# Performance work log

Hardware: AMD Instinct MI355X
Metric: run time of the kernel (lower is better)

## Reference

```python
import jax, jax.numpy as jnp
import numpy as np

D = 32   # input_dim == all hidden dims
L = 4    # number of GeneralizedRelationalConv layers
R = 36   # num_relation (incl. inverse relations)


def _bellmanford(edge_index, edge_type, h_index, r_index, num_nodes,
                 query_emb, rel_W, rel_b, conv_W, conv_b):
    """NBFNet Bellman-Ford pass: relation-conditioned conv with PNA aggregation."""
    B = r_index.shape[0]
    N = num_nodes
    E = edge_type.shape[0]
    d = query_emb.shape[1]

    query = query_emb[r_index]                                   # [B, d]
    # boundary condition: indicator embedding at the head node
    boundary = jnp.zeros((B, N, d), jnp.float32).at[jnp.arange(B), h_index].add(query)

    src, dst = edge_index[0], edge_index[1]
    # augment every node with a self-loop carrying the boundary message
    idx_aug = jnp.concatenate([dst, jnp.arange(N)])              # [E + N]
    deg = jax.ops.segment_sum(jnp.ones(E + N, jnp.float32), idx_aug, num_segments=N)  # >= 1
    dlog = jnp.log(deg)
    scale = dlog / jnp.mean(dlog)
    # PNA degree scalers: identity / amplification / attenuation
    scales = jnp.stack([jnp.ones_like(scale), scale, 1.0 / jnp.clip(scale, 1e-2)], axis=-1)  # [N, 3]

    x = boundary
    for l in range(L):
        # dependent relation embeddings: linear projection of the query
        rel = (query @ rel_W[l].T + rel_b[l]).reshape(B, R, d)   # [B, R, d]
        # distmult message: gather source state, modulate by edge relation
        msg = x[:, src, :] * rel[:, edge_type, :]                # [B, E, d]
        msg = jnp.concatenate([msg, boundary], axis=1)           # [B, E+N, d] incl. self-loops

        def agg(m):  # segment stats over destination nodes
            s = jax.ops.segment_sum(m, idx_aug, num_segments=N)
            sq = jax.ops.segment_sum(m * m, idx_aug, num_segments=N)
            mx = jax.ops.segment_max(m, idx_aug, num_segments=N)
            mn = jax.ops.segment_min(m, idx_aug, num_segments=N)
            return s, sq, mx, mn

        s, sq, mx, mn = jax.vmap(agg)(msg)                       # each [B, N, d]
        mean = s / deg[:, None]
        sq_mean = sq / deg[:, None]
        std = jnp.sqrt(jnp.clip(sq_mean - mean * mean, 1e-6))
        feats = jnp.stack([mean, mx, mn, std], axis=-1).reshape(B, N, 4 * d)
        update = (feats[..., None] * scales[None, :, None, :]).reshape(B, N, 12 * d)
        # combine: linear over cat(input, pna_update) then ReLU
        x = jax.nn.relu(jnp.concatenate([x, update], axis=-1) @ conv_W[l].T + conv_b[l])

    node_query = jnp.broadcast_to(query[:, None, :], (B, N, d))
    return jnp.concatenate([x, node_query], axis=-1)             # [B, N, 2d]


def setup_inputs() -> dict:
    key = jax.random.key(0)
    ks = jax.random.split(key, 10)
    N, E, B, K = 20000, 200000, 4, 32
    return {
        "edge_index": jax.random.randint(ks[0], (2, E), 0, N),
        "edge_type": jax.random.randint(ks[1], (E,), 0, R),
        "h_index": jax.random.randint(ks[2], (B,), 0, N),
        "t_index": jax.random.randint(ks[3], (B, K), 0, N),
        "r_index": jax.random.randint(ks[4], (B,), 0, R),
        "num_nodes": N,
        "query_emb": jax.random.normal(ks[5], (R, D), jnp.float32) * 0.1,
        "rel_W": jax.random.normal(ks[6], (L, R * D, D), jnp.float32) * 0.1,
        "rel_b": jnp.zeros((L, R * D), jnp.float32),
        "conv_W": jax.random.normal(ks[7], (L, D, 13 * D), jnp.float32) * 0.05,
        "conv_b": jnp.zeros((L, D), jnp.float32),
        "mlp_W1": jax.random.normal(ks[8], (2 * D, 2 * D), jnp.float32) * 0.1,
        "mlp_b1": jnp.zeros((2 * D,), jnp.float32),
        "mlp_W2": jax.random.normal(ks[9], (1, 2 * D), jnp.float32) * 0.1,
        "mlp_b2": jnp.zeros((1,), jnp.float32),
    }


def reference(edge_index, edge_type, h_index, t_index, r_index, num_nodes,
              query_emb, rel_W, rel_b, conv_W, conv_b,
              mlp_W1, mlp_b1, mlp_W2, mlp_b2):
    feature = _bellmanford(edge_index, edge_type, h_index, r_index, num_nodes,
                           query_emb, rel_W, rel_b, conv_W, conv_b)
    B = h_index.shape[0]
    f_t = feature[jnp.arange(B)[:, None], t_index]               # [B, K, 2d]
    h = jax.nn.relu(f_t @ mlp_W1.T + mlp_b1)
    score = (h @ mlp_W2.T + mlp_b2)[..., 0]                      # [B, K]
    return score
```

## Files before the change

kernel.cpp:

```cpp
#include <hip/hip_runtime.h>
#include <hip/hip_bf16.h>

#define N_NODES 20000
#define N_EDGES 200000
#define BB 4
#define KK 32
#define DD 32
#define RR 36
#define LL 4
#define NCHUNKS (N_NODES / 16)
#define NBLK 79

constexpr size_t OFF_X0   = 0;
constexpr size_t OFF_X1   = OFF_X0 + (size_t)BB * N_NODES * DD;
constexpr size_t OFF_RP   = OFF_X1 + (size_t)BB * N_NODES * DD;
constexpr size_t OFF_CUR  = OFF_RP + 20032;
constexpr size_t OFF_ES   = OFF_CUR + N_NODES;
constexpr size_t OFF_DEG  = OFF_ES + N_EDGES;
constexpr size_t OFF_SC   = OFF_DEG + N_NODES;
constexpr size_t OFF_INV  = OFF_SC + N_NODES;
constexpr size_t OFF_BS   = OFF_INV + N_NODES;
constexpr size_t OFF_BL   = OFF_BS + 128;
constexpr size_t OFF_BO   = OFF_BL + 128;
constexpr size_t OFF_MEAN = OFF_BO + 128;
constexpr size_t OFF_REL  = OFF_MEAN + 16;
constexpr size_t OFF_PW   = OFF_REL + (size_t)LL * RR * BB * DD;
constexpr size_t OFF_F    = OFF_PW + (size_t)LL * 16 * 832;


__global__ void k_init(const int* __restrict__ h_index, const int* __restrict__ r_index,
                       const float* __restrict__ query_emb, float* __restrict__ x0,
                       int* __restrict__ cursor) {
    int i = blockIdx.x * blockDim.x + threadIdx.x;
    int stride = gridDim.x * blockDim.x;
    for (int t = i; t < N_NODES; t += stride) cursor[t] = 0;
    for (int t = i; t < BB * N_NODES * DD; t += stride) {
        int b = t & 3; int d = (t >> 2) & 31; int n = t >> 7;
        float v = 0.f;
        if (n == h_index[b]) v = query_emb[r_index[b] * DD + d];
        x0[t] = v;
    }
}

__global__ void k_hist(const int* __restrict__ ei, int* __restrict__ cursor) {
    int e = blockIdx.x * blockDim.x + threadIdx.x;
    if (e < N_EDGES) atomicAdd(&cursor[ei[N_EDGES + e]], 1);
}

__global__ void k_part(const int* __restrict__ cursor, int* __restrict__ bsum,
                       float* __restrict__ blog) {
    __shared__ int si[256];
    __shared__ float sf2[256];
    int tid = threadIdx.x;
    int i = blockIdx.x * 256 + tid;
    int v = (i < N_NODES) ? cursor[i] : 0;
    float lg = (i < N_NODES) ? logf((float)(v + 1)) : 0.f;
    si[tid] = v; sf2[tid] = lg;
    __syncthreads();
    for (int off = 128; off > 0; off >>= 1) {
        if (tid < off) { si[tid] += si[tid + off]; sf2[tid] += sf2[tid + off]; }
        __syncthreads();
    }
    if (tid == 0) { bsum[blockIdx.x] = si[0]; blog[blockIdx.x] = sf2[0]; }
}

__global__ void k_scan2(const int* __restrict__ bsum, const float* __restrict__ blog,
                        int* __restrict__ boff, float* __restrict__ meanw) {
    __shared__ int si[128];
    __shared__ float sf2[128];
    int t = threadIdx.x;
    int v = (t < NBLK) ? bsum[t] : 0;
    float lg = (t < NBLK) ? blog[t] : 0.f;
    si[t] = v; sf2[t] = lg;
    __syncthreads();
    for (int off = 1; off < 128; off <<= 1) {
        int tv = (t >= off) ? si[t - off] : 0;
        float tf = (t >= off) ? sf2[t - off] : 0.f;
        __syncthreads();
        si[t] += tv; sf2[t] += tf;
        __syncthreads();
    }
    if (t < NBLK) boff[t] = si[t] - v;
    if (t == 127) meanw[0] = sf2[127] / (float)N_NODES;
}

__global__ void k_final(int* __restrict__ cursor, int* __restrict__ row_ptr,
                        const int* __restrict__ boff, const float* __restrict__ meanw,
                        float* __restrict__ rdeg, float* __restrict__ scale,
                        float* __restrict__ invs) {
    __shared__ int si[256];
    int tid = threadIdx.x;
    int i = blockIdx.x * 256 + tid;
    int v = (i < N_NODES) ? cursor[i] : 0;
    si[tid] = v;
    __syncthreads();
    for (int off = 1; off < 256; off <<= 1) {
        int tv = (tid >= off) ? si[tid - off] : 0;
        __syncthreads();
        si[tid] += tv;
        __syncthreads();
    }
    int rp = boff[blockIdx.x] + si[tid] - v;
    if (i < N_NODES) {
        row_ptr[i] = rp;
        cursor[i] = rp;
        float dg = (float)(v + 1);
        float sc = logf(dg) / meanw[0];
        rdeg[i] = 1.f / dg;
        scale[i] = sc;
        invs[i] = 1.f / fmaxf(sc, 0.01f);
    }
    if (i == 0) row_ptr[N_NODES] = N_EDGES;
}

__global__ void k_scatter(const int* __restrict__ ei, const int* __restrict__ et,
                          int* __restrict__ cursor, int* __restrict__ es) {
    int e = blockIdx.x * blockDim.x + threadIdx.x;
    if (e < N_EDGES) {
        int dnode = ei[N_EDGES + e];
        int p = atomicAdd(&cursor[dnode], 1);
        es[p] = ei[e] | (et[e] << 16);
    }
}

__global__ void k_prep_w(const float* __restrict__ query_emb, const int* __restrict__ r_index,
                         const float* __restrict__ rel_W, const float* __restrict__ rel_b,
                         const float* __restrict__ conv_W,
                         float* __restrict__ rel_all, float* __restrict__ pw) {
    int i = blockIdx.x * blockDim.x + threadIdx.x;
    const int NREL = LL * BB * RR * DD;
    if (i < NREL) {
        int d = i & 31;
        int ty = (i >> 5) % RR;
        int b = (i / (32 * RR)) & 3;
        int l = i / (32 * RR * BB);
        const float* q = query_emb + r_index[b] * DD;
        const float* w = rel_W + ((size_t)l * RR * DD + ty * DD + d) * DD;
        float acc = rel_b[l * RR * DD + ty * DD + d];
        #pragma unroll
        for (int k2 = 0; k2 < DD; ++k2) acc = fmaf(q[k2], w[k2], acc);
        rel_all[(((size_t)l * RR + ty) * DD + d) * BB + b] = acc;
    } else {
        int i2 = i - NREL;
        if (i2 >= LL * 16 * 832) return;
        int r = i2 % 832; int lw = i2 / 832;
        int w = lw & 15, l = lw >> 4;
        int o, col;
        if (r < 64) { col = r >> 1; o = w * 2 + (r & 1); }
        else {
            int r2 = r - 64;
            int jj = r2 / 24, rem = r2 % 24;
            int p = rem >> 1;
            o = w * 2 + (rem & 1);
            col = DD + (jj * 4 + p / 3) * 3 + (p % 3);
        }
        pw[i2] = conv_W[(size_t)(l * DD + o) * (13 * DD) + col];
    }
}

__launch_bounds__(256, 6)
__global__ void k_gather(const float* __restrict__ xin, float4* __restrict__ Fq,
                         const int* __restrict__ row_ptr, const int* __restrict__ es,
                         const float* __restrict__ rel_l, const float* __restrict__ rdeg,
                         const int* __restrict__ h_index, const int* __restrict__ r_index,
                         const float* __restrict__ query_emb) {
    __shared__ __align__(16) float s_rel[RR * BB * DD];
    const int tid = threadIdx.x;
    {
        const float4* p4 = (const float4*)rel_l;
        float4* s4 = (float4*)s_rel;
        for (int i = tid; i < RR * BB * DD / 4; i += 256) s4[i] = p4[i];
    }
    const int lane = tid & 63;
    const int d = lane & 31;
    const int par = lane >> 5;
    int hb[4]; float qv[4];
    #pragma unroll
    for (int b = 0; b < 4; ++b) {
        hb[b] = h_index[b];
        qv[b] = query_emb[r_index[b] * DD + d];
    }
    __syncthreads();

    const int nwaves = gridDim.x * 4;
    for (int n = blockIdx.x * 4 + (tid >> 6); n < N_NODES; n += nwaves) {
        float sa[4], sq[4], mx[4], mn[4];
        #pragma unroll
        for (int b = 0; b < 4; ++b) {
            float bv = (n == hb[b]) ? qv[b] : 0.f;
            float bs = par ? 0.f : bv;
            sa[b] = bs; sq[b] = bs * bv; mx[b] = bv; mn[b] = bv;
        }
        auto proc = [&](int ee) {
            int pk = es[ee];
            float4 xv = *(const float4*)(xin + ((size_t)(pk & 0xFFFF) * DD + d) * 4);
            float4 rv = *(const float4*)(s_rel + (((pk >> 16) * DD) + d) * 4);
            #pragma unroll
            for (int b = 0; b < 4; ++b) {
                float m = (&xv.x)[b] * (&rv.x)[b];
                sa[b] += m; sq[b] = fmaf(m, m, sq[b]);
                mx[b] = fmaxf(mx[b], m); mn[b] = fminf(mn[b], m);
            }
        };
        int e0 = row_ptr[n], e1 = row_ptr[n + 1];
        int e = e0 + par;
        for (; e + 6 < e1; e += 8) { proc(e); proc(e + 2); proc(e + 4); proc(e + 6); }
        for (; e < e1; e += 2) proc(e);
        #pragma unroll
        for (int b = 0; b < 4; ++b) {
            sa[b] += __shfl_xor(sa[b], 32);
            sq[b] += __shfl_xor(sq[b], 32);
            mx[b] = fmaxf(mx[b], __shfl_xor(mx[b], 32));
            mn[b] = fminf(mn[b], __shfl_xor(mn[b], 32));
        }
        float rd_ = rdeg[n];
        float mean[4], sd[4];
        #pragma unroll
        for (int b = 0; b < 4; ++b) {
            mean[b] = sa[b] * rd_;
            float sm = sq[b] * rd_;
            sd[b] = sqrtf(fmaxf(sm - mean[b] * mean[b], 1e-6f));
        }
        const int chunk = n >> 4, nl = n & 15;
        int tA = nl * 4 + par * 2;
        float4 fA, fB;
        fA.x = par ? mean[2] : mean[0]; fA.y = par ? mx[2] : mx[0];
        fA.z = par ? mn[2] : mn[0];     fA.w = par ? sd[2] : sd[0];
        fB.x = par ? mean[3] : mean[1]; fB.y = par ? mx[3] : mx[1];
        fB.z = par ? mn[3] : mn[1];     fB.w = par ? sd[3] : sd[1];
        Fq[(size_t)(chunk * 32 + d) * 64 + tA] = fA;
        Fq[(size_t)(chunk * 32 + d) * 64 + tA + 1] = fB;
    }
}

#define FMAB(CF, JJ) do {                                                      \
    _Pragma("unroll")                                                          \
    for (int p_ = 0; p_ < 12; ++p_) {                                          \
        const int f_ = p_ / 3, k_ = p_ % 3;                                    \
        float wlo_ = wfp[(JJ) * 24 + p_ * 2];                                  \
        float whi_ = wfp[(JJ) * 24 + p_ * 2 + 1];                              \
        _Pragma("unroll")                                                      \
        for (int cc_ = 0; cc_ < 5; ++cc_) {                                    \
            float cv_ = (&CF[cc_].x)[f_];                                      \
            y[cc_][k_][0] = fmaf(cv_, wlo_, y[cc_][k_][0]);                    \
            y[cc_][k_][1] = fmaf(cv_, whi_, y[cc_][k_][1]);                    \
        }                                                                      \
    }                                                                          \
} while (0)

#define LOADCF(CF, ROW) do {                                                   \
    _Pragma("unroll")                                                          \
    for (int cc_ = 0; cc_ < 5; ++cc_)                                          \
        CF[cc_] = Fq[(size_t)((set * 5 + cc_) * 32 + (ROW)) * 64 + lane];      \
} while (0)

__launch_bounds__(1024, 4)
__global__ void k_conv(const float* __restrict__ xin, float* __restrict__ xout,
                       const float4* __restrict__ Fq, const float* __restrict__ pw_l,
                       const float* __restrict__ scale, const float* __restrict__ invs,
                       const float* __restrict__ conv_b_l) {
    const int tid = threadIdx.x;
    const int wq = __builtin_amdgcn_readfirstlane(tid >> 6);
    const int lane = tid & 63;
    const float* wxp = pw_l + wq * 832;
    const float* wfp = wxp + 64;
    float bx = conv_b_l[wq * 2], by = conv_b_l[wq * 2 + 1];

    const int set = blockIdx.x;
    const int nl2 = lane >> 2, b2 = lane & 3;

    float y[5][3][2];
    #pragma unroll
    for (int cc = 0; cc < 5; ++cc) {
        y[cc][0][0] = bx; y[cc][0][1] = by;
        y[cc][1][0] = 0.f; y[cc][1][1] = 0.f;
        y[cc][2][0] = 0.f; y[cc][2][1] = 0.f;
    }

    #pragma unroll 2
    for (int jg = 0; jg < 8; ++jg) {
        float cxv[5][4];
        #pragma unroll
        for (int cc = 0; cc < 5; ++cc) {
            int n = (set * 5 + cc) * 16 + nl2;
            const float* xb = xin + (size_t)n * 128 + b2;
            #pragma unroll
            for (int dj = 0; dj < 4; ++dj)
                cxv[cc][dj] = xb[(jg * 4 + dj) * 4];
        }
        #pragma unroll
        for (int dj = 0; dj < 4; ++dj) {
            int j = jg * 4 + dj;
            float wlo = wxp[2 * j];
            float whi = wxp[2 * j + 1];
            #pragma unroll
            for (int cc = 0; cc < 5; ++cc) {
                float cv = cxv[cc][dj];
                y[cc][0][0] = fmaf(cv, wlo, y[cc][0][0]);
                y[cc][0][1] = fmaf(cv, whi, y[cc][0][1]);
            }
        }
    }

    float4 cf0[5], cf1[5], cf2[5], cf3[5];
    LOADCF(cf0, 0);
    LOADCF(cf1, 1);
    LOADCF(cf2, 2);
    #pragma unroll 1
    for (int jj = 0; jj < 32; jj += 4) {
        LOADCF(cf3, jj + 3); FMAB(cf0, jj);
        LOADCF(cf0, jj + 4); FMAB(cf1, jj + 1);
        LOADCF(cf1, jj + 5); FMAB(cf2, jj + 2);
        LOADCF(cf2, jj + 6); FMAB(cf3, jj + 3);
    }

    #pragma unroll
    for (int cc = 0; cc < 5; ++cc) {
        int n = (set * 5 + cc) * 16 + nl2;
        float scn = scale[n], ivn = invs[n];
        float* xo = xout + (size_t)n * 128 + b2;
        float v0 = fmaxf(0.f, y[cc][0][0] + scn * y[cc][1][0] + ivn * y[cc][2][0]);
        float v1 = fmaxf(0.f, y[cc][0][1] + scn * y[cc][1][1] + ivn * y[cc][2][1]);
        xo[(wq * 2) * 4] = v0;
        xo[(wq * 2 + 1) * 4] = v1;
    }
}

__global__ void k_score(const float* __restrict__ xL, const float* __restrict__ query_emb,
                        const int* __restrict__ r_index, const int* __restrict__ t_index,
                        const float* __restrict__ W1, const float* __restrict__ b1,
                        const float* __restrict__ W2, const float* __restrict__ b2,
                        float* __restrict__ out) {
    int bi = blockIdx.x;
    int b = bi >> 5, kk = bi & 31;
    int j = threadIdx.x;
    __shared__ float sf[64];
    int t = t_index[b * KK + kk];
    float f = (j < DD) ? xL[(size_t)t * 128 + j * 4 + b]
                       : query_emb[r_index[b] * DD + (j - DD)];
    sf[j] = f;
    __syncthreads();
    float acc = b1[j];
    #pragma unroll 8
    for (int i2 = 0; i2 < 64; ++i2) acc = fmaf(sf[i2], W1[j * 64 + i2], acc);
    float h = fmaxf(acc, 0.f);
    float prod = h * W2[j];
    #pragma unroll
    for (int off = 32; off > 0; off >>= 1) prod += __shfl_down(prod, off);
    if (j == 0) out[b * KK + kk] = prod + b2[0];
}

extern "C" void kernel_launch(void* const* d_in, const int* in_sizes, int n_in,
                              void* d_out, int out_size, void* d_ws, size_t ws_size,
                              hipStream_t stream) {
    const int* ei        = (const int*)d_in[0];
    const int* et        = (const int*)d_in[1];
    const int* h_index   = (const int*)d_in[2];
    const int* t_index   = (const int*)d_in[3];
    const int* r_index   = (const int*)d_in[4];
    const float* query_emb = (const float*)d_in[6];
    const float* rel_W   = (const float*)d_in[7];
    const float* rel_b   = (const float*)d_in[8];
    const float* conv_W  = (const float*)d_in[9];
    const float* conv_b  = (const float*)d_in[10];
    const float* W1      = (const float*)d_in[11];
    const float* b1      = (const float*)d_in[12];
    const float* W2      = (const float*)d_in[13];
    const float* b2      = (const float*)d_in[14];

    float* ws = (float*)d_ws;
    float* x0      = ws + OFF_X0;
    float* x1      = ws + OFF_X1;
    int*   row_ptr = (int*)(ws + OFF_RP);
    int*   cursor  = (int*)(ws + OFF_CUR);
    int*   es      = (int*)(ws + OFF_ES);
    float* rdeg    = ws + OFF_DEG;
    float* sc      = ws + OFF_SC;
    float* invs    = ws + OFF_INV;
    int*   bsum    = (int*)(ws + OFF_BS);
    float* blog    = ws + OFF_BL;
    int*   boff    = (int*)(ws + OFF_BO);
    float* meanw   = ws + OFF_MEAN;
    float* rel_all = ws + OFF_REL;
    float* pw      = ws + OFF_PW;
    float4* Fq     = (float4*)(ws + OFF_F);
    float* out     = (float*)d_out;

    k_init<<<1024, 256, 0, stream>>>(h_index, r_index, query_emb, x0, cursor);
    k_hist<<<(N_EDGES + 255) / 256, 256, 0, stream>>>(ei, cursor);
    k_part<<<NBLK, 256, 0, stream>>>(cursor, bsum, blog);
    k_scan2<<<1, 128, 0, stream>>>(bsum, blog, boff, meanw);
    k_final<<<NBLK, 256, 0, stream>>>(cursor, row_ptr, boff, meanw, rdeg, sc, invs);
    k_scatter<<<(N_EDGES + 255) / 256, 256, 0, stream>>>(ei, et, cursor, es);
    const int NPREP = LL * BB * RR * DD + LL * 16 * 832;
    k_prep_w<<<(NPREP + 255) / 256, 256, 0, stream>>>(query_emb, r_index, rel_W, rel_b,
                                                      conv_W, rel_all, pw);

    for (int l = 0; l < LL; ++l) {
        const float* xi = (l & 1) ? x1 : x0;
        float* xo = (l & 1) ? x0 : x1;
        k_gather<<<1536, 256, 0, stream>>>(xi, Fq, row_ptr, es,
                                           rel_all + (size_t)l * RR * BB * DD,
                                           rdeg, h_index, r_index, query_emb);
        k_conv<<<250, 1024, 0, stream>>>(xi, xo, Fq, pw + (size_t)l * 16 * 832,
                                         sc, invs, conv_b + l * DD);
    }

    k_score<<<BB * KK, 64, 0, stream>>>(x0, query_emb, r_index, t_index, W1, b1, W2, b2, out);
}
```

Before: 322.7 us.

## Retile conv kernel: 4 waves × 8 outputs per 16-node chunk

Restructures the dense conv kernel so each block covers one 16-node chunk with four waves, each computing 8 output channels. Previously a 1024-thread block covered 5 chunks with 16 waves of 2 outputs each. The weight packing in k_prep_w is reordered to match the new layout. This raises the FMA count per feature load and gives more, smaller blocks for better occupancy, at the cost of re-reading features across 4 waves instead of 16 per chunk and using fewer independent loads in flight.

```diff
diff --git a/kernel.cpp b/kernel.cpp
--- a/kernel.cpp
+++ b/kernel.cpp
@@ -25,7 +25,7 @@
 constexpr size_t OFF_MEAN = OFF_BO + 128;
 constexpr size_t OFF_REL  = OFF_MEAN + 16;
 constexpr size_t OFF_PW   = OFF_REL + (size_t)LL * RR * BB * DD;
-constexpr size_t OFF_F    = OFF_PW + (size_t)LL * 16 * 832;
+constexpr size_t OFF_F    = OFF_PW + (size_t)LL * 4 * 3328;
 
 
 __global__ void k_init(const int* __restrict__ h_index, const int* __restrict__ r_index,
@@ -142,17 +142,17 @@
         rel_all[(((size_t)l * RR + ty) * DD + d) * BB + b] = acc;
     } else {
         int i2 = i - NREL;
-        if (i2 >= LL * 16 * 832) return;
-        int r = i2 % 832; int lw = i2 / 832;
-        int w = lw & 15, l = lw >> 4;
+        if (i2 >= LL * 4 * 3328) return;
+        int r = i2 % 3328; int lg2 = i2 / 3328;
+        int og = lg2 & 3, l = lg2 >> 2;
         int o, col;
-        if (r < 64) { col = r >> 1; o = w * 2 + (r & 1); }
+        if (r < 256) { col = r >> 3; o = og * 8 + (r & 7); }
         else {
-            int r2 = r - 64;
-            int jj = r2 / 24, rem = r2 % 24;
-            int p = rem >> 1;
-            o = w * 2 + (rem & 1);
-            col = DD + (jj * 4 + p / 3) * 3 + (p % 3);
+            int r2 = r - 256;
+            int jj = r2 / 96, rem = r2 % 96;
+            int pf = rem >> 3;
+            o = og * 8 + (rem & 7);
+            col = DD + (jj * 4 + pf / 3) * 3 + (pf % 3);
         }
         pw[i2] = conv_W[(size_t)(l * DD + o) * (13 * DD) + col];
     }
@@ -233,96 +233,68 @@
     }
 }
 
-#define FMAB(CF, JJ) do {                                                      \
-    _Pragma("unroll")                                                          \
-    for (int p_ = 0; p_ < 12; ++p_) {                                          \
-        const int f_ = p_ / 3, k_ = p_ % 3;                                    \
-        float wlo_ = wfp[(JJ) * 24 + p_ * 2];                                  \
-        float whi_ = wfp[(JJ) * 24 + p_ * 2 + 1];                              \
-        _Pragma("unroll")                                                      \
-        for (int cc_ = 0; cc_ < 5; ++cc_) {                                    \
-            float cv_ = (&CF[cc_].x)[f_];                                      \
-            y[cc_][k_][0] = fmaf(cv_, wlo_, y[cc_][k_][0]);                    \
-            y[cc_][k_][1] = fmaf(cv_, whi_, y[cc_][k_][1]);                    \
-        }                                                                      \
-    }                                                                          \
-} while (0)
-
-#define LOADCF(CF, ROW) do {                                                   \
-    _Pragma("unroll")                                                          \
-    for (int cc_ = 0; cc_ < 5; ++cc_)                                          \
-        CF[cc_] = Fq[(size_t)((set * 5 + cc_) * 32 + (ROW)) * 64 + lane];      \
-} while (0)
-
-__launch_bounds__(1024, 4)
+__launch_bounds__(256, 6)
 __global__ void k_conv(const float* __restrict__ xin, float* __restrict__ xout,
                        const float4* __restrict__ Fq, const float* __restrict__ pw_l,
                        const float* __restrict__ scale, const float* __restrict__ invs,
                        const float* __restrict__ conv_b_l) {
     const int tid = threadIdx.x;
-    const int wq = __builtin_amdgcn_readfirstlane(tid >> 6);
+    const int og = __builtin_amdgcn_readfirstlane(tid >> 6);
     const int lane = tid & 63;
-    const float* wxp = pw_l + wq * 832;
-    const float* wfp = wxp + 64;
-    float bx = conv_b_l[wq * 2], by = conv_b_l[wq * 2 + 1];
-
-    const int set = blockIdx.x;
+    const int chunk = blockIdx.x;
+    const float* wxp = pw_l + og * 3328;
+    const float* wfp = wxp + 256;
+
     const int nl2 = lane >> 2, b2 = lane & 3;
-
-    float y[5][3][2];
+    const int n = chunk * 16 + nl2;
+
+    float y0[8], y1[8], y2[8];
     #pragma unroll
-    for (int cc = 0; cc < 5; ++cc) {
-        y[cc][0][0] = bx; y[cc][0][1] = by;
-        y[cc][1][0] = 0.f; y[cc][1][1] = 0.f;
-        y[cc][2][0] = 0.f; y[cc][2][1] = 0.f;
-    }
-
+    for (int oo = 0; oo < 8; ++oo) {
+        y0[oo] = conv_b_l[og * 8 + oo];
+        y1[oo] = 0.f;
+        y2[oo] = 0.f;
+    }
+
+    const float* xb = xin + (size_t)n * 128 + b2;
     #pragma unroll 2
     for (int jg = 0; jg < 8; ++jg) {
-        float cxv[5][4];
-        #pragma unroll
-        for (int cc = 0; cc < 5; ++cc) {
-            int n = (set * 5 + cc) * 16 + nl2;
-            const float* xb = xin + (size_t)n * 128 + b2;
-            #pragma unroll
-            for (int dj = 0; dj < 4; ++dj)
-                cxv[cc][dj] = xb[(jg * 4 + dj) * 4];
-        }
+        float cxv[4];
+        #pragma unroll
+        for (int dj = 0; dj < 4; ++dj) cxv[dj] = xb[(jg * 4 + dj) * 4];
         #pragma unroll
         for (int dj = 0; dj < 4; ++dj) {
-            int j = jg * 4 + dj;
-            float wlo = wxp[2 * j];
-            float whi = wxp[2 * j + 1];
-            #pragma unroll
-            for (int cc = 0; cc < 5; ++cc) {
-                float cv = cxv[cc][dj];
-                y[cc][0][0] = fmaf(cv, wlo, y[cc][0][0]);
-                y[cc][0][1] = fmaf(cv, whi, y[cc][0][1]);
-            }
-        }
-    }
-
-    float4 cf0[5], cf1[5], cf2[5], cf3[5];
-    LOADCF(cf0, 0);
-    LOADCF(cf1, 1);
-    LOADCF(cf2, 2);
+            const float* wp = wxp + (jg * 4 + dj) * 8;
+            #pragma unroll
+            for (int oo = 0; oo < 8; ++oo) y0[oo] = fmaf(cxv[dj], wp[oo], y0[oo]);
+        }
+    }
+
+    float4 fa = Fq[(size_t)(chunk * 32) * 64 + lane];
     #pragma unroll 1
-    for (int jj = 0; jj < 32; jj += 4) {
-        LOADCF(cf3, jj + 3); FMAB(cf0, jj);
-        LOADCF(cf0, jj + 4); FMAB(cf1, jj + 1);
-        LOADCF(cf1, jj + 5); FMAB(cf2, jj + 2);
-        LOADCF(cf2, jj + 6); FMAB(cf3, jj + 3);
-    }
-
+    for (int jj = 0; jj < 32; ++jj) {
+        float4 fb = Fq[(size_t)(chunk * 32 + jj + 1) * 64 + lane];
+        const float* wp = wfp + jj * 96;
+        #pragma unroll
+        for (int f = 0; f < 4; ++f) {
+            float cv = (&fa.x)[f];
+            const float* w8 = wp + f * 24;
+            #pragma unroll
+            for (int oo = 0; oo < 8; ++oo) y0[oo] = fmaf(cv, w8[oo], y0[oo]);
+            #pragma unroll
+            for (int oo = 0; oo < 8; ++oo) y1[oo] = fmaf(cv, w8[8 + oo], y1[oo]);
+            #pragma unroll
+            for (int oo = 0; oo < 8; ++oo) y2[oo] = fmaf(cv, w8[16 + oo], y2[oo]);
+        }
+        fa = fb;
+    }
+
+    float scn = scale[n], ivn = invs[n];
+    float* xo = xout + (size_t)n * 128 + b2;
     #pragma unroll
-    for (int cc = 0; cc < 5; ++cc) {
-        int n = (set * 5 + cc) * 16 + nl2;
-        float scn = scale[n], ivn = invs[n];
-        float* xo = xout + (size_t)n * 128 + b2;
-        float v0 = fmaxf(0.f, y[cc][0][0] + scn * y[cc][1][0] + ivn * y[cc][2][0]);
-        float v1 = fmaxf(0.f, y[cc][0][1] + scn * y[cc][1][1] + ivn * y[cc][2][1]);
-        xo[(wq * 2) * 4] = v0;
-        xo[(wq * 2 + 1) * 4] = v1;
+    for (int oo = 0; oo < 8; ++oo) {
+        float v = fmaxf(0.f, y0[oo] + scn * y1[oo] + ivn * y2[oo]);
+        xo[(og * 8 + oo) * 4] = v;
     }
 }
 
@@ -392,7 +364,7 @@
     k_scan2<<<1, 128, 0, stream>>>(bsum, blog, boff, meanw);
     k_final<<<NBLK, 256, 0, stream>>>(cursor, row_ptr, boff, meanw, rdeg, sc, invs);
     k_scatter<<<(N_EDGES + 255) / 256, 256, 0, stream>>>(ei, et, cursor, es);
-    const int NPREP = LL * BB * RR * DD + LL * 16 * 832;
+    const int NPREP = LL * BB * RR * DD + LL * 4 * 3328;
     k_prep_w<<<(NPREP + 255) / 256, 256, 0, stream>>>(query_emb, r_index, rel_W, rel_b,
                                                       conv_W, rel_all, pw);
 
@@ -402,8 +374,8 @@
         k_gather<<<1536, 256, 0, stream>>>(xi, Fq, row_ptr, es,
                                            rel_all + (size_t)l * RR * BB * DD,
                                            rdeg, h_index, r_index, query_emb);
-        k_conv<<<250, 1024, 0, stream>>>(xi, xo, Fq, pw + (size_t)l * 16 * 832,
-                                         sc, invs, conv_b + l * DD);
+        k_conv<<<NCHUNKS, 256, 0, stream>>>(xi, xo, Fq, pw + (size_t)l * 4 * 3328,
+                                            sc, invs, conv_b + l * DD);
     }
 
     k_score<<<BB * KK, 64, 0, stream>>>(x0, query_emb, r_index, t_index, W1, b1, W2, b2, out);
```

Measured after the change: 267.0 us (median of 2 runs). -17.3%, faster.
